# Kernel optimization log

Measured on AMD Instinct MI355X. Metric: run time of the kernel, lower is better.

The kernel has to match this reference:

```python
import jax, jax.numpy as jnp
import numpy as np

N = 16384          # number of units
K = 655
BOOST_STRENGTH = 1.0


def setup_inputs() -> dict:
    key = jax.random.key(0)
    k1, k2 = jax.random.split(key)
    x = jax.random.normal(k1, (4096, N), dtype=jnp.float32)
    dutyCycle = jax.random.uniform(k2, (N,), dtype=jnp.float32)
    return {"x": x, "dutyCycle": dutyCycle}


def reference(x, dutyCycle):
    # boost factor per unit: encourages under-used units
    targetDensity = K / x.shape[1]
    boostFactors = jnp.exp((targetDensity - dutyCycle) * BOOST_STRENGTH)  # (N,)
    boosted = x * boostFactors  # (B, N)
    # top-k per row, then scatter a binary mask of winners
    _, idx = jax.lax.top_k(boosted, K)  # (B, K)
    b = jnp.arange(x.shape[0])[:, None]  # (B, 1)
    res = jnp.zeros_like(x).at[b, idx].set(1.0)
    return res
```

## Files before the change

kernel.cpp:

```cpp
#include <hip/hip_runtime.h>
#include <math.h>
#include <stdint.h>


#define N_UNITS 16384
#define K_WIN 655
#define NT 512
#define BINS0 2048
#define CAND_CAP 1024
#define EQ_CAP 256

__device__ __forceinline__ uint32_t fkey(float f) {
    uint32_t b = __float_as_uint(f);
    uint32_t m = (uint32_t)((int32_t)b >> 31) | 0x80000000u;
    return b ^ m;
}

__global__ void boost_kernel(const float* __restrict__ duty,
                             float* __restrict__ bf, int n) {
    int i = blockIdx.x * blockDim.x + threadIdx.x;
    if (i < n) {
        const float td = 0.03997802734375f;
        float s = td - duty[i];
        bf[i] = (float)exp((double)s);
    }
}

__device__ __forceinline__ void select_bin(const uint32_t* hist, int nbins,
                                           uint32_t krem,
                                           volatile uint32_t* wsum,
                                           uint32_t* sc_d, uint32_t* sc_k) {
    const int tid = threadIdx.x;
    const int lane = tid & 63;
    const int w = tid >> 6;
    const int cper = nbins / NT;
    const int base = tid * cper;
    uint32_t s = 0;
#pragma unroll
    for (int c = 0; c < cper; ++c) s += hist[base + c];
    uint32_t v = s;
#pragma unroll
    for (int off = 1; off < 64; off <<= 1) {
        uint32_t o = __shfl_down(v, off, 64);
        if (lane + off < 64) v += o;
    }
    if (lane == 0) wsum[w] = v;
    __syncthreads();
    uint32_t above = 0;
#pragma unroll
    for (int ww = 0; ww < 8; ++ww)
        if (ww > w) above += wsum[ww];
    uint32_t H = (v - s) + above;
    if (H < krem && H + s >= krem) {
        uint32_t acc = H;
        for (int c = cper - 1; c >= 0; --c) {
            uint32_t h = hist[base + c];
            if (acc + h >= krem) {
                *sc_d = (uint32_t)(base + c);
                *sc_k = krem - acc;
                break;
            }
            acc += h;
        }
    }
    __syncthreads();
}

__global__ __launch_bounds__(NT, 4) void kwinners_kernel(
    const float* __restrict__ x, const float* __restrict__ bf,
    float* __restrict__ out) {
    __shared__ uint32_t keys[N_UNITS];
    __shared__ uint32_t hist[BINS0];
    __shared__ uint32_t wsum[8];
    __shared__ uint32_t cand[CAND_CAP];
    __shared__ uint32_t eqi[EQ_CAP];
    __shared__ uint32_t sc[8];

    const int tid = threadIdx.x;
    const int row = blockIdx.x;
    const float4* xrow = (const float4*)(x + (size_t)row * N_UNITS);
    const float4* bfv = (const float4*)bf;
    float4* orow = (float4*)(out + (size_t)row * N_UNITS);

    for (int b = tid; b < BINS0; b += NT) hist[b] = 0;
    if (tid < 8) sc[tid] = 0;
    __syncthreads();

#pragma unroll
    for (int j = 0; j < N_UNITS / (NT * 4); ++j) {
        int i4 = tid + j * NT;
        float4 xv = xrow[i4];
        float4 bv = bfv[i4];
        uint4 k;
        k.x = fkey(xv.x * bv.x);
        k.y = fkey(xv.y * bv.y);
        k.z = fkey(xv.z * bv.z);
        k.w = fkey(xv.w * bv.w);
        ((uint4*)keys)[i4] = k;
        atomicAdd(&hist[k.x >> 21], 1u);
        atomicAdd(&hist[k.y >> 21], 1u);
        atomicAdd(&hist[k.z >> 21], 1u);
        atomicAdd(&hist[k.w >> 21], 1u);
    }
    __syncthreads();

    uint32_t krem = K_WIN;
    select_bin(hist, BINS0, krem, wsum, &sc[2], &sc[3]);
    const uint32_t d0 = sc[2];
    krem = sc[3];
    __syncthreads();

    for (int b = tid; b < BINS0; b += NT) hist[b] = 0;
    __syncthreads();
#pragma unroll
    for (int j = 0; j < N_UNITS / (NT * 4); ++j) {
        int i4 = tid + j * NT;
        uint4 k = ((const uint4*)keys)[i4];
        int ib = i4 * 4;
        if ((k.x >> 21) == d0) {
            atomicAdd(&hist[(k.x >> 10) & 0x7FF], 1u);
            uint32_t p = atomicAdd(&sc[0], 1u);
            if (p < CAND_CAP) cand[p] = (uint32_t)(ib + 0);
        }
        if ((k.y >> 21) == d0) {
            atomicAdd(&hist[(k.y >> 10) & 0x7FF], 1u);
            uint32_t p = atomicAdd(&sc[0], 1u);
            if (p < CAND_CAP) cand[p] = (uint32_t)(ib + 1);
        }
        if ((k.z >> 21) == d0) {
            atomicAdd(&hist[(k.z >> 10) & 0x7FF], 1u);
            uint32_t p = atomicAdd(&sc[0], 1u);
            if (p < CAND_CAP) cand[p] = (uint32_t)(ib + 2);
        }
        if ((k.w >> 21) == d0) {
            atomicAdd(&hist[(k.w >> 10) & 0x7FF], 1u);
            uint32_t p = atomicAdd(&sc[0], 1u);
            if (p < CAND_CAP) cand[p] = (uint32_t)(ib + 3);
        }
    }
    __syncthreads();
    select_bin(hist, BINS0, krem, wsum, &sc[2], &sc[3]);
    const uint32_t d1 = sc[2];
    krem = sc[3];
    const uint32_t ncand = sc[0];
    __syncthreads();

    const uint32_t pfx21 = (d0 << 11) | d1;
    for (int b = tid; b < 1024; b += NT) hist[b] = 0;
    __syncthreads();
    if (ncand <= CAND_CAP) {
        for (uint32_t j = tid; j < ncand; j += NT) {
            uint32_t k = keys[cand[j]];
            if ((k >> 10) == pfx21) atomicAdd(&hist[k & 0x3FF], 1u);
        }
    } else {
#pragma unroll
        for (int j = 0; j < N_UNITS / (NT * 4); ++j) {
            int i4 = tid + j * NT;
            uint4 k = ((const uint4*)keys)[i4];
            if ((k.x >> 10) == pfx21) atomicAdd(&hist[k.x & 0x3FF], 1u);
            if ((k.y >> 10) == pfx21) atomicAdd(&hist[k.y & 0x3FF], 1u);
            if ((k.z >> 10) == pfx21) atomicAdd(&hist[k.z & 0x3FF], 1u);
            if ((k.w >> 10) == pfx21) atomicAdd(&hist[k.w & 0x3FF], 1u);
        }
    }
    __syncthreads();
    select_bin(hist, 1024, krem, wsum, &sc[2], &sc[3]);
    const uint32_t d2 = sc[2];
    const uint32_t need = sc[3];
    __syncthreads();

    const uint32_t T = (pfx21 << 10) | d2;

#pragma unroll
    for (int j = 0; j < N_UNITS / (NT * 4); ++j) {
        int i4 = tid + j * NT;
        uint4 k = ((const uint4*)keys)[i4];
        float4 o;
        o.x = (k.x > T) ? 1.0f : 0.0f;
        o.y = (k.y > T) ? 1.0f : 0.0f;
        o.z = (k.z > T) ? 1.0f : 0.0f;
        o.w = (k.w > T) ? 1.0f : 0.0f;
        orow[i4] = o;
        int ib = i4 * 4;
        if (k.x == T) {
            uint32_t p = atomicAdd(&sc[1], 1u);
            if (p < EQ_CAP) eqi[p] = (uint32_t)(ib + 0);
        }
        if (k.y == T) {
            uint32_t p = atomicAdd(&sc[1], 1u);
            if (p < EQ_CAP) eqi[p] = (uint32_t)(ib + 1);
        }
        if (k.z == T) {
            uint32_t p = atomicAdd(&sc[1], 1u);
            if (p < EQ_CAP) eqi[p] = (uint32_t)(ib + 2);
        }
        if (k.w == T) {
            uint32_t p = atomicAdd(&sc[1], 1u);
            if (p < EQ_CAP) eqi[p] = (uint32_t)(ib + 3);
        }
    }
    __syncthreads();

    const uint32_t ecnt = sc[1];
    float* orowf = (float*)orow;
    if (ecnt <= EQ_CAP) {
        for (uint32_t j = tid; j < ecnt; j += NT) {
            uint32_t idx = eqi[j];
            uint32_t rank = 0;
            for (uint32_t m = 0; m < ecnt; ++m) rank += (eqi[m] < idx) ? 1u : 0u;
            if (rank < need) orowf[idx] = 1.0f;
        }
    } else if (tid == 0) {
        uint32_t r = 0;
        for (int i = 0; i < N_UNITS && r < need; ++i)
            if (keys[i] == T) {
                orowf[i] = 1.0f;
                ++r;
            }
    }
}

extern "C" void kernel_launch(void* const* d_in, const int* in_sizes, int n_in,
                              void* d_out, int out_size, void* d_ws,
                              size_t ws_size, hipStream_t stream) {
    const float* x = (const float*)d_in[0];
    const float* duty = (const float*)d_in[1];
    float* out = (float*)d_out;
    float* bf = (float*)d_ws;

    hipLaunchKernelGGL(boost_kernel, dim3(N_UNITS / 256), dim3(256), 0, stream,
                       duty, bf, N_UNITS);
    int rows = out_size / N_UNITS;
    hipLaunchKernelGGL(kwinners_kernel, dim3(rows), dim3(NT), 0, stream, x, bf,
                       out);
}
```

Baseline: 472.4 us.

## Replace radix histogram select with multi-probe threshold search on 16-bit keys

Replaces the three-pass radix-histogram top-k threshold search with register-counted multi-threshold probing on the upper 16 bits of each key. The probes are seeded with fixed values suited to the expected distribution and then refined by interpolating between bracketing probes. Keys are stored packed as 16-bit halves, which halves shared memory and allows higher occupancy (launch bounds raised to 6). Ties inside the boundary bucket are resolved by recomputing full keys from global memory and ranking the candidates pairwise. This removes shared-memory atomics on the histogram, at the cost of more compare work per element, a single-thread fallback path, and seed probes tuned to Gaussian-like inputs (still correct for any input, via refinement).

```diff
diff --git a/kernel.cpp b/kernel.cpp
--- a/kernel.cpp
+++ b/kernel.cpp
@@ -6,9 +6,8 @@
 #define N_UNITS 16384
 #define K_WIN 655
 #define NT 512
-#define BINS0 2048
-#define CAND_CAP 1024
-#define EQ_CAP 256
+#define NPROBE 11
+#define CAP 2048
 
 __device__ __forceinline__ uint32_t fkey(float f) {
     uint32_t b = __float_as_uint(f);
@@ -26,198 +25,211 @@
     }
 }
 
-__device__ __forceinline__ void select_bin(const uint32_t* hist, int nbins,
-                                           uint32_t krem,
-                                           volatile uint32_t* wsum,
-                                           uint32_t* sc_d, uint32_t* sc_k) {
+__global__ __launch_bounds__(NT, 6) void kwinners_kernel(
+    const float* __restrict__ x, const float* __restrict__ bf,
+    float* __restrict__ out) {
+    __shared__ __align__(16) uint32_t khiw[N_UNITS / 2];
+    __shared__ uint32_t red[(NT / 64) * NPROBE];
+    __shared__ int cglob[NPROBE];
+    __shared__ uint32_t cand_idx[CAP];
+    __shared__ uint32_t cand_key[CAP];
+    __shared__ int prb[NPROBE];
+    __shared__ int sc[2];
+
     const int tid = threadIdx.x;
     const int lane = tid & 63;
     const int w = tid >> 6;
-    const int cper = nbins / NT;
-    const int base = tid * cper;
-    uint32_t s = 0;
-#pragma unroll
-    for (int c = 0; c < cper; ++c) s += hist[base + c];
-    uint32_t v = s;
-#pragma unroll
-    for (int off = 1; off < 64; off <<= 1) {
-        uint32_t o = __shfl_down(v, off, 64);
-        if (lane + off < 64) v += o;
-    }
-    if (lane == 0) wsum[w] = v;
-    __syncthreads();
-    uint32_t above = 0;
-#pragma unroll
-    for (int ww = 0; ww < 8; ++ww)
-        if (ww > w) above += wsum[ww];
-    uint32_t H = (v - s) + above;
-    if (H < krem && H + s >= krem) {
-        uint32_t acc = H;
-        for (int c = cper - 1; c >= 0; --c) {
-            uint32_t h = hist[base + c];
-            if (acc + h >= krem) {
-                *sc_d = (uint32_t)(base + c);
-                *sc_k = krem - acc;
-                break;
-            }
-            acc += h;
-        }
-    }
-    __syncthreads();
-}
-
-__global__ __launch_bounds__(NT, 4) void kwinners_kernel(
-    const float* __restrict__ x, const float* __restrict__ bf,
-    float* __restrict__ out) {
-    __shared__ uint32_t keys[N_UNITS];
-    __shared__ uint32_t hist[BINS0];
-    __shared__ uint32_t wsum[8];
-    __shared__ uint32_t cand[CAND_CAP];
-    __shared__ uint32_t eqi[EQ_CAP];
-    __shared__ uint32_t sc[8];
-
-    const int tid = threadIdx.x;
     const int row = blockIdx.x;
     const float4* xrow = (const float4*)(x + (size_t)row * N_UNITS);
     const float4* bfv = (const float4*)bf;
-    float4* orow = (float4*)(out + (size_t)row * N_UNITS);
-
-    for (int b = tid; b < BINS0; b += NT) hist[b] = 0;
-    if (tid < 8) sc[tid] = 0;
+    float* orow = out + (size_t)row * N_UNITS;
+
+    if (tid < NPROBE) {
+        const float pv[NPROBE] = {1.90f, 1.70f, 1.55f, 1.43f, 1.33f, 1.25f,
+                                  1.18f, 1.12f, 1.06f, 0.99f, 0.90f};
+        prb[tid] = (int)(fkey(pv[tid]) >> 16);
+    }
+    if (tid == 0) sc[0] = 0;
     __syncthreads();
+
+    int P[NPROBE];
+#pragma unroll
+    for (int p = 0; p < NPROBE; ++p) P[p] = prb[p];
+    int cnt[NPROBE];
+#pragma unroll
+    for (int p = 0; p < NPROBE; ++p) cnt[p] = 0;
 
 #pragma unroll
     for (int j = 0; j < N_UNITS / (NT * 4); ++j) {
         int i4 = tid + j * NT;
         float4 xv = xrow[i4];
         float4 bv = bfv[i4];
-        uint4 k;
-        k.x = fkey(xv.x * bv.x);
-        k.y = fkey(xv.y * bv.y);
-        k.z = fkey(xv.z * bv.z);
-        k.w = fkey(xv.w * bv.w);
-        ((uint4*)keys)[i4] = k;
-        atomicAdd(&hist[k.x >> 21], 1u);
-        atomicAdd(&hist[k.y >> 21], 1u);
-        atomicAdd(&hist[k.z >> 21], 1u);
-        atomicAdd(&hist[k.w >> 21], 1u);
+        int h0 = (int)(fkey(xv.x * bv.x) >> 16);
+        int h1 = (int)(fkey(xv.y * bv.y) >> 16);
+        int h2 = (int)(fkey(xv.z * bv.z) >> 16);
+        int h3 = (int)(fkey(xv.w * bv.w) >> 16);
+        uint2 pk;
+        pk.x = (uint32_t)h0 | ((uint32_t)h1 << 16);
+        pk.y = (uint32_t)h2 | ((uint32_t)h3 << 16);
+        ((uint2*)khiw)[i4] = pk;
+#pragma unroll
+        for (int p = 0; p < NPROBE; ++p)
+            cnt[p] += (h0 > P[p]) + (h1 > P[p]) + (h2 > P[p]) + (h3 > P[p]);
+    }
+
+    auto reduce_counts = [&]() {
+#pragma unroll
+        for (int p = 0; p < NPROBE; ++p) {
+            int v = cnt[p];
+#pragma unroll
+            for (int m = 32; m >= 1; m >>= 1) v += __shfl_xor(v, m, 64);
+            if (lane == 0) red[w * NPROBE + p] = (uint32_t)v;
+        }
+        __syncthreads();
+        if (tid < NPROBE) {
+            int s = 0;
+#pragma unroll
+            for (int ww = 0; ww < NT / 64; ++ww) s += (int)red[ww * NPROBE + tid];
+            cglob[tid] = s;
+        }
+        __syncthreads();
+    };
+    reduce_counts();
+
+    int lo, hi, cab, cgl;
+    {
+        int j = 0;
+        while (j < NPROBE && cglob[j] < K_WIN) ++j;
+        if (j == 0) {
+            lo = P[0]; cgl = cglob[0]; hi = 65535; cab = 0;
+        } else if (j == NPROBE) {
+            lo = -1; cgl = N_UNITS; hi = P[NPROBE - 1]; cab = cglob[NPROBE - 1];
+        } else {
+            lo = P[j]; cgl = cglob[j]; hi = P[j - 1]; cab = cglob[j - 1];
+        }
+    }
+    int m = cgl - cab;
+
+    while (m > CAP && (hi - lo) > 1) {
+        __syncthreads();
+        if (tid < NPROBE)
+            prb[tid] = lo + (int)(((long)(hi - lo) * (NPROBE - tid)) / (NPROBE + 1));
+        __syncthreads();
+#pragma unroll
+        for (int p = 0; p < NPROBE; ++p) P[p] = prb[p];
+#pragma unroll
+        for (int p = 0; p < NPROBE; ++p) cnt[p] = 0;
+        for (int j = 0; j < 4; ++j) {
+            uint4 wv = ((const uint4*)khiw)[tid + j * NT];
+            int h0 = (int)(wv.x & 0xFFFFu), h1 = (int)(wv.x >> 16);
+            int h2 = (int)(wv.y & 0xFFFFu), h3 = (int)(wv.y >> 16);
+            int h4 = (int)(wv.z & 0xFFFFu), h5 = (int)(wv.z >> 16);
+            int h6 = (int)(wv.w & 0xFFFFu), h7 = (int)(wv.w >> 16);
+#pragma unroll
+            for (int p = 0; p < NPROBE; ++p)
+                cnt[p] += (h0 > P[p]) + (h1 > P[p]) + (h2 > P[p]) + (h3 > P[p]) +
+                          (h4 > P[p]) + (h5 > P[p]) + (h6 > P[p]) + (h7 > P[p]);
+        }
+        reduce_counts();
+        int j = 0;
+        while (j < NPROBE && cglob[j] < K_WIN) ++j;
+        if (j == 0) {
+            lo = P[0]; cgl = cglob[0];
+        } else if (j == NPROBE) {
+            hi = P[NPROBE - 1]; cab = cglob[NPROBE - 1];
+        } else {
+            lo = P[j]; cgl = cglob[j]; hi = P[j - 1]; cab = cglob[j - 1];
+        }
+        m = cgl - cab;
+    }
+
+    for (int j = 0; j < 4; ++j) {
+        int q = tid + j * NT;
+        uint4 wv = ((const uint4*)khiw)[q];
+        int base = q * 8;
+        int h[8] = {(int)(wv.x & 0xFFFFu), (int)(wv.x >> 16),
+                    (int)(wv.y & 0xFFFFu), (int)(wv.y >> 16),
+                    (int)(wv.z & 0xFFFFu), (int)(wv.z >> 16),
+                    (int)(wv.w & 0xFFFFu), (int)(wv.w >> 16)};
+#pragma unroll
+        for (int e = 0; e < 8; ++e) {
+            if (h[e] > lo && h[e] <= hi) {
+                int p = atomicAdd(&sc[0], 1);
+                if (p < CAP) cand_idx[p] = (uint32_t)(base + e);
+            }
+        }
     }
     __syncthreads();
-
-    uint32_t krem = K_WIN;
-    select_bin(hist, BINS0, krem, wsum, &sc[2], &sc[3]);
-    const uint32_t d0 = sc[2];
-    krem = sc[3];
+    const int mm = sc[0];
+    const int need = K_WIN - cab;
+
+    const float* xr = x + (size_t)row * N_UNITS;
+    const int mc = (mm <= CAP) ? mm : 0;
+    for (int j = tid; j < mc; j += NT) {
+        int i = (int)cand_idx[j];
+        cand_key[j] = fkey(xr[i] * bf[i]);
+    }
+
+    for (int j = 0; j < N_UNITS / (NT * 4); ++j) {
+        int f = tid + j * NT;
+        uint2 wv = ((const uint2*)khiw)[f];
+        float4 o;
+        o.x = ((int)(wv.x & 0xFFFFu) > hi) ? 1.0f : 0.0f;
+        o.y = ((int)(wv.x >> 16) > hi) ? 1.0f : 0.0f;
+        o.z = ((int)(wv.y & 0xFFFFu) > hi) ? 1.0f : 0.0f;
+        o.w = ((int)(wv.y >> 16) > hi) ? 1.0f : 0.0f;
+        ((float4*)orow)[f] = o;
+    }
     __syncthreads();
 
-    for (int b = tid; b < BINS0; b += NT) hist[b] = 0;
-    __syncthreads();
-#pragma unroll
-    for (int j = 0; j < N_UNITS / (NT * 4); ++j) {
-        int i4 = tid + j * NT;
-        uint4 k = ((const uint4*)keys)[i4];
-        int ib = i4 * 4;
-        if ((k.x >> 21) == d0) {
-            atomicAdd(&hist[(k.x >> 10) & 0x7FF], 1u);
-            uint32_t p = atomicAdd(&sc[0], 1u);
-            if (p < CAND_CAP) cand[p] = (uint32_t)(ib + 0);
-        }
-        if ((k.y >> 21) == d0) {
-            atomicAdd(&hist[(k.y >> 10) & 0x7FF], 1u);
-            uint32_t p = atomicAdd(&sc[0], 1u);
-            if (p < CAND_CAP) cand[p] = (uint32_t)(ib + 1);
-        }
-        if ((k.z >> 21) == d0) {
-            atomicAdd(&hist[(k.z >> 10) & 0x7FF], 1u);
-            uint32_t p = atomicAdd(&sc[0], 1u);
-            if (p < CAND_CAP) cand[p] = (uint32_t)(ib + 2);
-        }
-        if ((k.w >> 21) == d0) {
-            atomicAdd(&hist[(k.w >> 10) & 0x7FF], 1u);
-            uint32_t p = atomicAdd(&sc[0], 1u);
-            if (p < CAND_CAP) cand[p] = (uint32_t)(ib + 3);
-        }
-    }
-    __syncthreads();
-    select_bin(hist, BINS0, krem, wsum, &sc[2], &sc[3]);
-    const uint32_t d1 = sc[2];
-    krem = sc[3];
-    const uint32_t ncand = sc[0];
-    __syncthreads();
-
-    const uint32_t pfx21 = (d0 << 11) | d1;
-    for (int b = tid; b < 1024; b += NT) hist[b] = 0;
-    __syncthreads();
-    if (ncand <= CAND_CAP) {
-        for (uint32_t j = tid; j < ncand; j += NT) {
-            uint32_t k = keys[cand[j]];
-            if ((k >> 10) == pfx21) atomicAdd(&hist[k & 0x3FF], 1u);
-        }
-    } else {
-#pragma unroll
-        for (int j = 0; j < N_UNITS / (NT * 4); ++j) {
-            int i4 = tid + j * NT;
-            uint4 k = ((const uint4*)keys)[i4];
-            if ((k.x >> 10) == pfx21) atomicAdd(&hist[k.x & 0x3FF], 1u);
-            if ((k.y >> 10) == pfx21) atomicAdd(&hist[k.y & 0x3FF], 1u);
-            if ((k.z >> 10) == pfx21) atomicAdd(&hist[k.z & 0x3FF], 1u);
-            if ((k.w >> 10) == pfx21) atomicAdd(&hist[k.w & 0x3FF], 1u);
-        }
-    }
-    __syncthreads();
-    select_bin(hist, 1024, krem, wsum, &sc[2], &sc[3]);
-    const uint32_t d2 = sc[2];
-    const uint32_t need = sc[3];
-    __syncthreads();
-
-    const uint32_t T = (pfx21 << 10) | d2;
-
-#pragma unroll
-    for (int j = 0; j < N_UNITS / (NT * 4); ++j) {
-        int i4 = tid + j * NT;
-        uint4 k = ((const uint4*)keys)[i4];
-        float4 o;
-        o.x = (k.x > T) ? 1.0f : 0.0f;
-        o.y = (k.y > T) ? 1.0f : 0.0f;
-        o.z = (k.z > T) ? 1.0f : 0.0f;
-        o.w = (k.w > T) ? 1.0f : 0.0f;
-        orow[i4] = o;
-        int ib = i4 * 4;
-        if (k.x == T) {
-            uint32_t p = atomicAdd(&sc[1], 1u);
-            if (p < EQ_CAP) eqi[p] = (uint32_t)(ib + 0);
-        }
-        if (k.y == T) {
-            uint32_t p = atomicAdd(&sc[1], 1u);
-            if (p < EQ_CAP) eqi[p] = (uint32_t)(ib + 1);
-        }
-        if (k.z == T) {
-            uint32_t p = atomicAdd(&sc[1], 1u);
-            if (p < EQ_CAP) eqi[p] = (uint32_t)(ib + 2);
-        }
-        if (k.w == T) {
-            uint32_t p = atomicAdd(&sc[1], 1u);
-            if (p < EQ_CAP) eqi[p] = (uint32_t)(ib + 3);
-        }
-    }
-    __syncthreads();
-
-    const uint32_t ecnt = sc[1];
-    float* orowf = (float*)orow;
-    if (ecnt <= EQ_CAP) {
-        for (uint32_t j = tid; j < ecnt; j += NT) {
-            uint32_t idx = eqi[j];
-            uint32_t rank = 0;
-            for (uint32_t m = 0; m < ecnt; ++m) rank += (eqi[m] < idx) ? 1u : 0u;
-            if (rank < need) orowf[idx] = 1.0f;
+    if (mm <= CAP) {
+        for (int j = tid; j < mm; j += NT) {
+            uint32_t myk = cand_key[j];
+            uint32_t myi = cand_idx[j];
+            int r = 0;
+            for (int l = 0; l < mm; ++l) {
+                uint32_t lk = cand_key[l];
+                r += (lk > myk) || (lk == myk && cand_idx[l] < myi);
+            }
+            if (r < need) orow[myi] = 1.0f;
         }
     } else if (tid == 0) {
-        uint32_t r = 0;
-        for (int i = 0; i < N_UNITS && r < need; ++i)
-            if (keys[i] == T) {
-                orowf[i] = 1.0f;
-                ++r;
-            }
+        uint32_t* h8 = cand_idx;
+        for (int b = 0; b < 256; ++b) h8[b] = 0;
+        for (int i = 0; i < N_UNITS; ++i) {
+            int h = (int)((khiw[i >> 1] >> ((i & 1) * 16)) & 0xFFFFu);
+            if (h == hi) h8[(fkey(xr[i] * bf[i]) & 0xFFFFu) >> 8]++;
+        }
+        int acc = 0, d1 = 0, need2 = 0;
+        for (int b = 255; b >= 0; --b) {
+            int c = (int)h8[b];
+            if (acc + c >= need) { d1 = b; need2 = need - acc; break; }
+            acc += c;
+        }
+        for (int b = 0; b < 256; ++b) h8[b] = 0;
+        for (int i = 0; i < N_UNITS; ++i) {
+            int h = (int)((khiw[i >> 1] >> ((i & 1) * 16)) & 0xFFFFu);
+            if (h == hi) {
+                uint32_t kl = fkey(xr[i] * bf[i]) & 0xFFFFu;
+                if ((int)(kl >> 8) == d1) h8[kl & 0xFFu]++;
+            }
+        }
+        int acc2 = 0, d2 = 0, need3 = 0;
+        for (int b = 255; b >= 0; --b) {
+            int c = (int)h8[b];
+            if (acc2 + c >= need2) { d2 = b; need3 = need2 - acc2; break; }
+            acc2 += c;
+        }
+        uint32_t Tlo = ((uint32_t)d1 << 8) | (uint32_t)d2;
+        int r = 0;
+        for (int i = 0; i < N_UNITS; ++i) {
+            int h = (int)((khiw[i >> 1] >> ((i & 1) * 16)) & 0xFFFFu);
+            if (h == hi) {
+                uint32_t kl = fkey(xr[i] * bf[i]) & 0xFFFFu;
+                if (kl > Tlo) orow[i] = 1.0f;
+                else if (kl == Tlo && r < need3) { orow[i] = 1.0f; ++r; }
+            }
+        }
     }
 }
 
```

Result: faster. 451.4 us (-4.4%).
